# Performance work log

Measured on AMD Instinct MI355X. Metric: run time of the kernel, lower is better.

Reference implementation:

```python
import jax, jax.numpy as jnp
import numpy as np
from jax import lax
from jax.scipy.special import logsumexp

B, T, C = 512, 512, 64


def setup_inputs() -> dict:
    key = jax.random.key(0)
    k1, k2, k3, k4, k5 = jax.random.split(key, 5)
    emissions = jax.random.normal(k1, (B, T, C), dtype=jnp.float32)
    tags = jax.random.randint(k2, (B, T), 0, C, dtype=jnp.int32)
    mask = jnp.ones((B, T), dtype=jnp.int32)
    transitions = jax.random.normal(k3, (C, C), dtype=jnp.float32)
    start_transitions = jax.random.normal(k4, (C,), dtype=jnp.float32)
    end_transitions = jax.random.normal(k5, (C,), dtype=jnp.float32)
    return {"emissions": emissions, "tags": tags, "mask": mask,
            "transitions": transitions, "start_transitions": start_transitions,
            "end_transitions": end_transitions}


def _log_partition(emissions, maskb, transitions, start_transitions, end_transitions):
    # forward algorithm: lp [B,C] carried over T-1 steps
    lp0 = start_transitions[None, :] + emissions[:, 0]  # [B,C]

    def step(lp, xs):
        emit_t, mask_t = xs  # [B,C], [B]
        # score[b,i,j] = lp[b,i] + trans[i,j] + emit[b,j]
        score = lp[:, :, None] + transitions[None, :, :] + emit_t[:, None, :]
        lp_next = logsumexp(score, axis=1)  # [B,C]
        lp = jnp.where(mask_t[:, None], lp_next, lp)
        return lp, None

    xs = (jnp.swapaxes(emissions[:, 1:], 0, 1), jnp.swapaxes(maskb[:, 1:], 0, 1))
    lp, _ = lax.scan(step, lp0, xs)
    return logsumexp(lp + end_transitions[None, :], axis=1)  # [B]


def _joint_score(emissions, tags, mask, maskb, transitions, start_transitions, end_transitions):
    b_idx = jnp.arange(emissions.shape[0])
    score0 = start_transitions[tags[:, 0]] + emissions[b_idx, 0, tags[:, 0]]  # [B]
    trans = transitions[tags[:, :-1], tags[:, 1:]]  # [B,T-1]
    emit = jnp.take_along_axis(emissions, tags[:, :, None], axis=2)[:, :, 0]  # [B,T]
    step_scores = jnp.where(maskb[:, 1:], trans + emit[:, 1:], 0.0)
    last_idx = jnp.sum(mask, axis=1).astype(jnp.int32) - 1
    last_tags = tags[b_idx, last_idx]
    return score0 + jnp.sum(step_scores, axis=1) + end_transitions[last_tags]


def reference(emissions, tags, mask, transitions, start_transitions, end_transitions):
    maskb = mask.astype(bool)
    log_denominator = _log_partition(emissions, maskb, transitions, start_transitions, end_transitions)
    log_numerator = _joint_score(emissions, tags, mask, maskb, transitions, start_transitions, end_transitions)
    return jnp.mean(log_denominator - log_numerator)
```

## Files before the change

kernel.cpp:

```cpp
#include <hip/hip_runtime.h>

#define Bn 512
#define Tn 512
#define Cn 64


template <int CTRL>
__device__ __forceinline__ float fmax_dpp(const float v) {
    const int o = __builtin_amdgcn_update_dpp(__float_as_int(v), __float_as_int(v),
                                              CTRL, 0xF, 0xF, false);
    return fmaxf(v, __int_as_float(o));
}

__device__ __forceinline__ float wave_max64(float v) {
    v = fmax_dpp<0x0B1>(v);
    v = fmax_dpp<0x04E>(v);
    v = fmax_dpp<0x141>(v);
    v = fmax_dpp<0x140>(v);
    v = fmax_dpp<0x142>(v);
    v = fmax_dpp<0x143>(v);
    return __int_as_float(__builtin_amdgcn_readlane(__float_as_int(v), 63));
}

__device__ __forceinline__ float bcast_dot64(const float a, const float* __restrict__ w) {
    const int ai = __float_as_int(a);
    float acc0 = 0.f, acc1 = 0.f, acc2 = 0.f, acc3 = 0.f;
#pragma unroll
    for (int i = 0; i < Cn; i += 4) {
        const float b0 = __int_as_float(__builtin_amdgcn_ds_bpermute(4 * (i + 0), ai));
        const float b1 = __int_as_float(__builtin_amdgcn_ds_bpermute(4 * (i + 1), ai));
        const float b2 = __int_as_float(__builtin_amdgcn_ds_bpermute(4 * (i + 2), ai));
        const float b3 = __int_as_float(__builtin_amdgcn_ds_bpermute(4 * (i + 3), ai));
        acc0 = fmaf(b0, w[i + 0], acc0);
        acc1 = fmaf(b1, w[i + 1], acc1);
        acc2 = fmaf(b2, w[i + 2], acc2);
        acc3 = fmaf(b3, w[i + 3], acc3);
    }
    return (acc0 + acc1) + (acc2 + acc3);
}

__global__ __launch_bounds__(64, 1) void crf_half_kernel(
    const float* __restrict__ emissions,
    const int*   __restrict__ tags,
    const int*   __restrict__ mask,
    const float* __restrict__ transitions,
    const float* __restrict__ start_t,
    const float* __restrict__ end_t,
    float*       __restrict__ ws_alpha,
    float*       __restrict__ ws_beta,
    float*       __restrict__ ws_lsF,
    float*       __restrict__ ws_lsB,
    float*       __restrict__ ws_num)
{
    const int  blk = blockIdx.x;
    const bool fwd = blk < Bn;
    const int  bt  = blk & (Bn - 1);
    const int  j   = threadIdx.x;

    const float* em  = emissions + (size_t)bt * Tn * Cn + j;
    const float* em0 = emissions + (size_t)bt * Tn * Cn;
    const int*   mk  = mask + bt * Tn;
    const int*   tg  = tags + bt * Tn;

    if (fwd) {
        float nsum = 0.f;
        int   mcnt = 0;
        for (int t = j; t < Tn; t += 64) {
            const int tag_t = tg[t];
            const int m_t   = mk[t];
            mcnt += m_t;
            if (t >= 1 && m_t) {
                const int tag_p = tg[t - 1];
                nsum += transitions[tag_p * Cn + tag_t] + em0[t * Cn + tag_t];
            }
        }
#pragma unroll
        for (int off = 32; off > 0; off >>= 1) {
            nsum += __shfl_xor(nsum, off, 64);
            mcnt += __shfl_xor(mcnt, off, 64);
        }

        float w[Cn];
#pragma unroll
        for (int i = 0; i < Cn; ++i) w[i] = __expf(transitions[i * Cn + j]);
#pragma unroll
        for (int i = 0; i < Cn; ++i) asm volatile("" : "+v"(w[i]));

        float lp0 = start_t[j] + em[0];
        const float m0 = wave_max64(lp0);
        float log_scale = m0;
        float a_self = __expf(lp0 - m0);
        float c_pend = 1.0f;

        float cur_e[4];
        int   cur_m[4];
#pragma unroll
        for (int k = 0; k < 4; ++k) {
            cur_e[k] = em[(size_t)(1 + k) * Cn];
            cur_m[k] = mk[1 + k];
        }

        for (int g = 0; g < 64; ++g) {
            float nxt_e[4];
            int   nxt_m[4];
#pragma unroll
            for (int k = 0; k < 4; ++k) {
                const int t = 4 * g + 5 + k;
                nxt_e[k] = em[(size_t)t * Cn];
                nxt_m[k] = mk[t];
            }
            float ex[4];
#pragma unroll
            for (int k = 0; k < 4; ++k) ex[k] = __expf(cur_e[k]);

#pragma unroll
            for (int k = 0; k < 4; ++k) {
                float s = bcast_dot64(a_self, w) * ex[k];
                if (!cur_m[k]) s = a_self;
                if (k == 0) {
                    s *= c_pend;
                    c_pend = 1.0f;
                }
                if (k == 3) {
                    const float mx = wave_max64(s);
                    c_pend = __builtin_amdgcn_rcpf(mx);
                    log_scale += __logf(mx);
                }
                a_self = s;
            }
#pragma unroll
            for (int k = 0; k < 4; ++k) {
                cur_e[k] = nxt_e[k];
                cur_m[k] = nxt_m[k];
            }
        }

        a_self *= c_pend;
        ws_alpha[bt * Cn + j] = a_self;
        if (j == 0) {
            ws_lsF[bt] = log_scale;
            const int t0 = tg[0];
            const int tl = tg[mcnt - 1];
            ws_num[bt] = start_t[t0] + em0[t0] + nsum + end_t[tl];
        }
    } else {
        float w[Cn];
#pragma unroll
        for (int i = 0; i < Cn; ++i) w[i] = __expf(transitions[j * Cn + i]);
#pragma unroll
        for (int i = 0; i < Cn; ++i) asm volatile("" : "+v"(w[i]));

        float lp0 = end_t[j];
        const float m0 = wave_max64(lp0);
        float log_scale = m0;
        float b_self = __expf(lp0 - m0);
        float c_pend = 1.0f;

        float cur_e[4];
        int   cur_m[4];
#pragma unroll
        for (int k = 0; k < 4; ++k) {
            const int u = Tn - 1 - k;
            cur_e[k] = em[(size_t)u * Cn];
            cur_m[k] = mk[u];
        }

        for (int g = 0; g < 64; ++g) {
            float nxt_e[4];
            int   nxt_m[4];
#pragma unroll
            for (int k = 0; k < 4; ++k) {
                const int u = Tn - 5 - 4 * g - k;
                nxt_e[k] = em[(size_t)u * Cn];
                nxt_m[k] = mk[u];
            }
            float ex[4];
#pragma unroll
            for (int k = 0; k < 4; ++k) ex[k] = __expf(cur_e[k]);

#pragma unroll
            for (int k = 0; k < 4; ++k) {
                const int s_idx = 4 * g + k;
                if (s_idx < Tn / 2 - 1) {
                    const float wval = b_self * ex[k];
                    float s = bcast_dot64(wval, w);
                    if (!cur_m[k]) s = b_self;
                    if (k == 0) {
                        s *= c_pend;
                        c_pend = 1.0f;
                    }
                    if (k == 3) {
                        const float mx = wave_max64(s);
                        c_pend = __builtin_amdgcn_rcpf(mx);
                        log_scale += __logf(mx);
                    }
                    b_self = s;
                }
            }
#pragma unroll
            for (int k = 0; k < 4; ++k) {
                cur_e[k] = nxt_e[k];
                cur_m[k] = nxt_m[k];
            }
        }

        b_self *= c_pend;
        ws_beta[bt * Cn + j] = b_self;
        if (j == 0) ws_lsB[bt] = log_scale;
    }
}

__global__ __launch_bounds__(1024) void crf_combine_kernel(
    const float* __restrict__ ws_alpha,
    const float* __restrict__ ws_beta,
    const float* __restrict__ ws_lsF,
    const float* __restrict__ ws_lsB,
    const float* __restrict__ ws_num,
    float*       __restrict__ out)
{
    const int wv = threadIdx.x >> 6;
    const int j  = threadIdx.x & 63;
    const int bt = blockIdx.x * 16 + wv;

    __shared__ float part[16];

    float v = ws_alpha[bt * Cn + j] * ws_beta[bt * Cn + j];
#pragma unroll
    for (int off = 32; off > 0; off >>= 1) v += __shfl_xor(v, off, 64);
    if (j == 0) {
        part[wv] = ws_lsF[bt] + ws_lsB[bt] + __logf(v) - ws_num[bt];
    }
    __syncthreads();
    if (threadIdx.x < 64) {
        float p = (j < 16) ? part[j] : 0.f;
#pragma unroll
        for (int off = 32; off > 0; off >>= 1) p += __shfl_xor(p, off, 64);
        if (j == 0) atomicAdd(out, p * (1.0f / Bn));
    }
}

__global__ void crf_zero_kernel(float* out) { out[0] = 0.f; }

extern "C" void kernel_launch(void* const* d_in, const int* in_sizes, int n_in,
                              void* d_out, int out_size, void* d_ws, size_t ws_size,
                              hipStream_t stream)
{
    const float* emissions   = (const float*)d_in[0];
    const int*   tags        = (const int*)d_in[1];
    const int*   mask        = (const int*)d_in[2];
    const float* transitions = (const float*)d_in[3];
    const float* start_t     = (const float*)d_in[4];
    const float* end_t       = (const float*)d_in[5];

    float* ws       = (float*)d_ws;
    float* ws_alpha = ws;
    float* ws_beta  = ws_alpha + Bn * Cn;
    float* ws_lsF   = ws_beta + Bn * Cn;
    float* ws_lsB   = ws_lsF + Bn;
    float* ws_num   = ws_lsB + Bn;

    crf_zero_kernel<<<1, 1, 0, stream>>>((float*)d_out);
    crf_half_kernel<<<2 * Bn, Cn, 0, stream>>>(emissions, tags, mask, transitions,
                                               start_t, end_t,
                                               ws_alpha, ws_beta, ws_lsF, ws_lsB, ws_num);
    crf_combine_kernel<<<Bn / 16, 1024, 0, stream>>>(ws_alpha, ws_beta, ws_lsF, ws_lsB,
                                                     ws_num, (float*)d_out);
}
```

Before: 171.3 us.

## Replace bpermute broadcast dot with DPP row-rotate systolic matvec and fold zero kernel

Swaps the 64 ds_bpermute broadcasts per step of the 64x64 matvec for a DPP row-rotate scheme. Each lane rotates its value within 16-lane rows, and three extra cross-row copies come from swizzle and shfl_xor. Transition weights are exp'd into LDS and gathered per lane in the matching permuted order. The separate zero-init kernel is also folded into the main kernel. This targets LDS-permute latency on the serial recurrence, at the cost of a more intricate weight layout that has to match the DPP/swizzle lane mapping exactly.

```diff
diff --git a/kernel.cpp b/kernel.cpp
--- a/kernel.cpp
+++ b/kernel.cpp
@@ -22,21 +22,60 @@
     return __int_as_float(__builtin_amdgcn_readlane(__float_as_int(v), 63));
 }
 
-__device__ __forceinline__ float bcast_dot64(const float a, const float* __restrict__ w) {
-    const int ai = __float_as_int(a);
-    float acc0 = 0.f, acc1 = 0.f, acc2 = 0.f, acc3 = 0.f;
-#pragma unroll
-    for (int i = 0; i < Cn; i += 4) {
-        const float b0 = __int_as_float(__builtin_amdgcn_ds_bpermute(4 * (i + 0), ai));
-        const float b1 = __int_as_float(__builtin_amdgcn_ds_bpermute(4 * (i + 1), ai));
-        const float b2 = __int_as_float(__builtin_amdgcn_ds_bpermute(4 * (i + 2), ai));
-        const float b3 = __int_as_float(__builtin_amdgcn_ds_bpermute(4 * (i + 3), ai));
-        acc0 = fmaf(b0, w[i + 0], acc0);
-        acc1 = fmaf(b1, w[i + 1], acc1);
-        acc2 = fmaf(b2, w[i + 2], acc2);
-        acc3 = fmaf(b3, w[i + 3], acc3);
-    }
-    return (acc0 + acc1) + (acc2 + acc3);
+template <int CTRL>
+__device__ __forceinline__ float dppf(const float v) {
+    return __int_as_float(__builtin_amdgcn_update_dpp(
+        __float_as_int(v), __float_as_int(v), CTRL, 0xF, 0xF, false));
+}
+
+__device__ __forceinline__ void phase_acc(const float vp, const float* __restrict__ wp,
+                                          float* __restrict__ A) {
+    A[0] = fmaf(vp,              wp[0],  A[0]);
+    A[1] = fmaf(dppf<0x121>(vp), wp[1],  A[1]);
+    A[2] = fmaf(dppf<0x122>(vp), wp[2],  A[2]);
+    A[3] = fmaf(dppf<0x123>(vp), wp[3],  A[3]);
+    A[4] = fmaf(dppf<0x124>(vp), wp[4],  A[4]);
+    A[5] = fmaf(dppf<0x125>(vp), wp[5],  A[5]);
+    A[6] = fmaf(dppf<0x126>(vp), wp[6],  A[6]);
+    A[7] = fmaf(dppf<0x127>(vp), wp[7],  A[7]);
+    A[0] = fmaf(dppf<0x128>(vp), wp[8],  A[0]);
+    A[1] = fmaf(dppf<0x129>(vp), wp[9],  A[1]);
+    A[2] = fmaf(dppf<0x12A>(vp), wp[10], A[2]);
+    A[3] = fmaf(dppf<0x12B>(vp), wp[11], A[3]);
+    A[4] = fmaf(dppf<0x12C>(vp), wp[12], A[4]);
+    A[5] = fmaf(dppf<0x12D>(vp), wp[13], A[5]);
+    A[6] = fmaf(dppf<0x12E>(vp), wp[14], A[6]);
+    A[7] = fmaf(dppf<0x12F>(vp), wp[15], A[7]);
+}
+
+__device__ __forceinline__ float systolic_dot(const float v, const float* __restrict__ w) {
+    const float v16 = __int_as_float(__builtin_amdgcn_ds_swizzle(__float_as_int(v), 0x401F));
+    const float v32 = __shfl_xor(v, 32, 64);
+    const float v48 = __int_as_float(__builtin_amdgcn_ds_swizzle(__float_as_int(v32), 0x401F));
+
+    float A[8];
+    A[0] = v               * w[0];
+    A[1] = dppf<0x121>(v)  * w[1];
+    A[2] = dppf<0x122>(v)  * w[2];
+    A[3] = dppf<0x123>(v)  * w[3];
+    A[4] = dppf<0x124>(v)  * w[4];
+    A[5] = dppf<0x125>(v)  * w[5];
+    A[6] = dppf<0x126>(v)  * w[6];
+    A[7] = dppf<0x127>(v)  * w[7];
+    A[0] = fmaf(dppf<0x128>(v), w[8],  A[0]);
+    A[1] = fmaf(dppf<0x129>(v), w[9],  A[1]);
+    A[2] = fmaf(dppf<0x12A>(v), w[10], A[2]);
+    A[3] = fmaf(dppf<0x12B>(v), w[11], A[3]);
+    A[4] = fmaf(dppf<0x12C>(v), w[12], A[4]);
+    A[5] = fmaf(dppf<0x12D>(v), w[13], A[5]);
+    A[6] = fmaf(dppf<0x12E>(v), w[14], A[6]);
+    A[7] = fmaf(dppf<0x12F>(v), w[15], A[7]);
+
+    phase_acc(v16, w + 16, A);
+    phase_acc(v32, w + 32, A);
+    phase_acc(v48, w + 48, A);
+
+    return ((A[0] + A[1]) + (A[2] + A[3])) + ((A[4] + A[5]) + (A[6] + A[7]));
 }
 
 __global__ __launch_bounds__(64, 1) void crf_half_kernel(
@@ -50,17 +89,45 @@
     float*       __restrict__ ws_beta,
     float*       __restrict__ ws_lsF,
     float*       __restrict__ ws_lsB,
-    float*       __restrict__ ws_num)
+    float*       __restrict__ ws_num,
+    float*       __restrict__ out)
 {
     const int  blk = blockIdx.x;
     const bool fwd = blk < Bn;
     const int  bt  = blk & (Bn - 1);
     const int  j   = threadIdx.x;
 
+    if (blk == 0 && j == 0) out[0] = 0.f;
+
     const float* em  = emissions + (size_t)bt * Tn * Cn + j;
     const float* em0 = emissions + (size_t)bt * Tn * Cn;
     const int*   mk  = mask + bt * Tn;
     const int*   tg  = tags + bt * Tn;
+
+    __shared__ float lW[Cn * Cn];
+#pragma unroll 8
+    for (int i = 0; i < Cn; ++i)
+        lW[i * Cn + j] = __expf(transitions[i * Cn + j]);
+    __builtin_amdgcn_wave_barrier();
+
+    float w[Cn];
+    if (fwd) {
+#pragma unroll
+        for (int p = 0; p < 4; ++p)
+#pragma unroll
+            for (int r = 0; r < 16; ++r) {
+                const int i = ((j & 48) ^ (p << 4)) | ((j + r) & 15);
+                w[p * 16 + r] = lW[i * Cn + j];
+            }
+    } else {
+#pragma unroll
+        for (int p = 0; p < 4; ++p)
+#pragma unroll
+            for (int r = 0; r < 16; ++r) {
+                const int i = ((j & 48) ^ (p << 4)) | ((j + r) & 15);
+                w[p * 16 + r] = lW[j * Cn + i];
+            }
+    }
 
     if (fwd) {
         float nsum = 0.f;
@@ -80,12 +147,6 @@
             mcnt += __shfl_xor(mcnt, off, 64);
         }
 
-        float w[Cn];
-#pragma unroll
-        for (int i = 0; i < Cn; ++i) w[i] = __expf(transitions[i * Cn + j]);
-#pragma unroll
-        for (int i = 0; i < Cn; ++i) asm volatile("" : "+v"(w[i]));
-
         float lp0 = start_t[j] + em[0];
         const float m0 = wave_max64(lp0);
         float log_scale = m0;
@@ -115,7 +176,7 @@
 
 #pragma unroll
             for (int k = 0; k < 4; ++k) {
-                float s = bcast_dot64(a_self, w) * ex[k];
+                float s = systolic_dot(a_self, w) * ex[k];
                 if (!cur_m[k]) s = a_self;
                 if (k == 0) {
                     s *= c_pend;
@@ -144,12 +205,6 @@
             ws_num[bt] = start_t[t0] + em0[t0] + nsum + end_t[tl];
         }
     } else {
-        float w[Cn];
-#pragma unroll
-        for (int i = 0; i < Cn; ++i) w[i] = __expf(transitions[j * Cn + i]);
-#pragma unroll
-        for (int i = 0; i < Cn; ++i) asm volatile("" : "+v"(w[i]));
-
         float lp0 = end_t[j];
         const float m0 = wave_max64(lp0);
         float log_scale = m0;
@@ -183,7 +238,7 @@
                 const int s_idx = 4 * g + k;
                 if (s_idx < Tn / 2 - 1) {
                     const float wval = b_self * ex[k];
-                    float s = bcast_dot64(wval, w);
+                    float s = systolic_dot(wval, w);
                     if (!cur_m[k]) s = b_self;
                     if (k == 0) {
                         s *= c_pend;
@@ -239,8 +294,6 @@
     }
 }
 
-__global__ void crf_zero_kernel(float* out) { out[0] = 0.f; }
-
 extern "C" void kernel_launch(void* const* d_in, const int* in_sizes, int n_in,
                               void* d_out, int out_size, void* d_ws, size_t ws_size,
                               hipStream_t stream)
@@ -259,10 +312,10 @@
     float* ws_lsB   = ws_lsF + Bn;
     float* ws_num   = ws_lsB + Bn;
 
-    crf_zero_kernel<<<1, 1, 0, stream>>>((float*)d_out);
     crf_half_kernel<<<2 * Bn, Cn, 0, stream>>>(emissions, tags, mask, transitions,
                                                start_t, end_t,
-                                               ws_alpha, ws_beta, ws_lsF, ws_lsB, ws_num);
+                                               ws_alpha, ws_beta, ws_lsF, ws_lsB, ws_num,
+                                               (float*)d_out);
     crf_combine_kernel<<<Bn / 16, 1024, 0, stream>>>(ws_alpha, ws_beta, ws_lsF, ws_lsB,
                                                      ws_num, (float*)d_out);
 }
```

Result: slower. 199.9 us (+16.7%).

## Split CRF recursion across two waves with LDS broadcast and halved dot products

Applied to the files above, without the earlier changes.

Each sequence block now uses 128 threads (two waves) instead of one. Each lane owns one output state and half of the 64-term reduction, and the partial sums are combined with a cross-half shuffle. The previous state vector goes through a double-buffered shared-memory array read as float4, replacing 64 ds_bpermute broadcasts per step. The per-group rescale max is computed from that buffered vector, and the zero-init kernel is folded into the main kernel. The trade-off is a __syncthreads barrier on every time step and twice the thread count per block.

```diff
diff --git a/kernel.cpp b/kernel.cpp
--- a/kernel.cpp
+++ b/kernel.cpp
@@ -4,6 +4,8 @@
 #define Tn 512
 #define Cn 64
 
+
+typedef float f4 __attribute__((ext_vector_type(4)));
 
 template <int CTRL>
 __device__ __forceinline__ float fmax_dpp(const float v) {
@@ -22,24 +24,47 @@
     return __int_as_float(__builtin_amdgcn_readlane(__float_as_int(v), 63));
 }
 
-__device__ __forceinline__ float bcast_dot64(const float a, const float* __restrict__ w) {
-    const int ai = __float_as_int(a);
-    float acc0 = 0.f, acc1 = 0.f, acc2 = 0.f, acc3 = 0.f;
-#pragma unroll
-    for (int i = 0; i < Cn; i += 4) {
-        const float b0 = __int_as_float(__builtin_amdgcn_ds_bpermute(4 * (i + 0), ai));
-        const float b1 = __int_as_float(__builtin_amdgcn_ds_bpermute(4 * (i + 1), ai));
-        const float b2 = __int_as_float(__builtin_amdgcn_ds_bpermute(4 * (i + 2), ai));
-        const float b3 = __int_as_float(__builtin_amdgcn_ds_bpermute(4 * (i + 3), ai));
-        acc0 = fmaf(b0, w[i + 0], acc0);
-        acc1 = fmaf(b1, w[i + 1], acc1);
-        acc2 = fmaf(b2, w[i + 2], acc2);
-        acc3 = fmaf(b3, w[i + 3], acc3);
-    }
-    return (acc0 + acc1) + (acc2 + acc3);
-}
-
-__global__ __launch_bounds__(64, 1) void crf_half_kernel(
+#define READ_BC(rb)                                                        \
+    const f4* ap_ = (const f4*)(&abuf[(rb)][h << 5]);                      \
+    const f4 b0_ = ap_[0], b1_ = ap_[1], b2_ = ap_[2], b3_ = ap_[3],       \
+             b4_ = ap_[4], b5_ = ap_[5], b6_ = ap_[6], b7_ = ap_[7];
+
+#define MAX_FROM_BC(dst)                                                   \
+    float dst;                                                             \
+    {                                                                      \
+        f4 t0_ = __builtin_elementwise_max(b0_, b1_);                      \
+        f4 t1_ = __builtin_elementwise_max(b2_, b3_);                      \
+        f4 t2_ = __builtin_elementwise_max(b4_, b5_);                      \
+        f4 t3_ = __builtin_elementwise_max(b6_, b7_);                      \
+        t0_ = __builtin_elementwise_max(t0_, t1_);                         \
+        t2_ = __builtin_elementwise_max(t2_, t3_);                         \
+        t0_ = __builtin_elementwise_max(t0_, t2_);                         \
+        dst = fmaxf(fmaxf(t0_.x, t0_.y), fmaxf(t0_.z, t0_.w));             \
+    }
+
+#define DOT_FROM_BC(dst)                                                   \
+    float dst;                                                             \
+    {                                                                      \
+        float a0_ = b0_.x * wreg[0],  a1_ = b0_.y * wreg[1];               \
+        float a2_ = b0_.z * wreg[2],  a3_ = b0_.w * wreg[3];               \
+        a0_ = fmaf(b1_.x, wreg[4],  a0_); a1_ = fmaf(b1_.y, wreg[5],  a1_);\
+        a2_ = fmaf(b1_.z, wreg[6],  a2_); a3_ = fmaf(b1_.w, wreg[7],  a3_);\
+        a0_ = fmaf(b2_.x, wreg[8],  a0_); a1_ = fmaf(b2_.y, wreg[9],  a1_);\
+        a2_ = fmaf(b2_.z, wreg[10], a2_); a3_ = fmaf(b2_.w, wreg[11], a3_);\
+        a0_ = fmaf(b3_.x, wreg[12], a0_); a1_ = fmaf(b3_.y, wreg[13], a1_);\
+        a2_ = fmaf(b3_.z, wreg[14], a2_); a3_ = fmaf(b3_.w, wreg[15], a3_);\
+        a0_ = fmaf(b4_.x, wreg[16], a0_); a1_ = fmaf(b4_.y, wreg[17], a1_);\
+        a2_ = fmaf(b4_.z, wreg[18], a2_); a3_ = fmaf(b4_.w, wreg[19], a3_);\
+        a0_ = fmaf(b5_.x, wreg[20], a0_); a1_ = fmaf(b5_.y, wreg[21], a1_);\
+        a2_ = fmaf(b5_.z, wreg[22], a2_); a3_ = fmaf(b5_.w, wreg[23], a3_);\
+        a0_ = fmaf(b6_.x, wreg[24], a0_); a1_ = fmaf(b6_.y, wreg[25], a1_);\
+        a2_ = fmaf(b6_.z, wreg[26], a2_); a3_ = fmaf(b6_.w, wreg[27], a3_);\
+        a0_ = fmaf(b7_.x, wreg[28], a0_); a1_ = fmaf(b7_.y, wreg[29], a1_);\
+        a2_ = fmaf(b7_.z, wreg[30], a2_); a3_ = fmaf(b7_.w, wreg[31], a3_);\
+        dst = (a0_ + a1_) + (a2_ + a3_);                                   \
+    }
+
+__global__ __launch_bounds__(128) void crf_half_kernel(
     const float* __restrict__ emissions,
     const int*   __restrict__ tags,
     const int*   __restrict__ mask,
@@ -50,165 +75,178 @@
     float*       __restrict__ ws_beta,
     float*       __restrict__ ws_lsF,
     float*       __restrict__ ws_lsB,
-    float*       __restrict__ ws_num)
+    float*       __restrict__ ws_num,
+    float*       __restrict__ out)
 {
-    const int  blk = blockIdx.x;
-    const bool fwd = blk < Bn;
-    const int  bt  = blk & (Bn - 1);
-    const int  j   = threadIdx.x;
-
-    const float* em  = emissions + (size_t)bt * Tn * Cn + j;
+    const int  blk  = blockIdx.x;
+    const bool fwd  = blk < Bn;
+    const int  bt   = blk & (Bn - 1);
+    const int  tid  = threadIdx.x;
+    const int  wv   = tid >> 6;
+    const int  l    = tid & 63;
+    const int  h    = l >> 5;
+    const int  ownj = (wv << 5) | (l & 31);
+
+    if (blk == 0 && tid == 0) out[0] = 0.f;
+
+    __shared__ __align__(16) float abuf[2][Cn];
+
+    const float* em  = emissions + (size_t)bt * Tn * Cn + ownj;
     const float* em0 = emissions + (size_t)bt * Tn * Cn;
     const int*   mk  = mask + bt * Tn;
     const int*   tg  = tags + bt * Tn;
 
+    float wreg[32];
     if (fwd) {
-        float nsum = 0.f;
-        int   mcnt = 0;
-        for (int t = j; t < Tn; t += 64) {
-            const int tag_t = tg[t];
-            const int m_t   = mk[t];
-            mcnt += m_t;
-            if (t >= 1 && m_t) {
-                const int tag_p = tg[t - 1];
-                nsum += transitions[tag_p * Cn + tag_t] + em0[t * Cn + tag_t];
-            }
+#pragma unroll
+        for (int m = 0; m < 32; ++m)
+            wreg[m] = __expf(transitions[(h * 32 + m) * Cn + ownj]);
+    } else {
+#pragma unroll
+        for (int m = 0; m < 32; ++m)
+            wreg[m] = __expf(transitions[ownj * Cn + h * 32 + m]);
+    }
+
+    float log_scale, self;
+
+    if (fwd) {
+        const float lp_l = start_t[l] + em0[l];
+        const float m0   = wave_max64(lp_l);
+        log_scale = m0;
+        self = __expf(start_t[ownj] + em0[ownj] - m0);
+
+        abuf[0][ownj] = self;
+        __syncthreads();
+
+        float cE[4]; int cM[4];
+#pragma unroll
+        for (int k = 0; k < 4; ++k) { cE[k] = em[(size_t)(1 + k) * Cn]; cM[k] = mk[1 + k]; }
+
+#pragma unroll 1
+        for (int g = 0; g < 64; ++g) {
+            float nE[4]; int nM[4];
+#pragma unroll
+            for (int k = 0; k < 4; ++k) {
+                const int t = 4 * g + 5 + k;
+                nE[k] = em[(size_t)t * Cn]; nM[k] = mk[t];
+            }
+            float ex[4];
+#pragma unroll
+            for (int k = 0; k < 4; ++k) ex[k] = __expf(cE[k]);
+
+#pragma unroll
+            for (int k = 0; k < 4; ++k) {
+                const int rb = k & 1;
+                READ_BC(rb);
+                float c_ = 1.0f;
+                if (k == 0 && g > 0) {
+                    MAX_FROM_BC(mxl_);
+                    const float mx_ = fmaxf(mxl_, __shfl_xor(mxl_, 32, 64));
+                    c_ = __builtin_amdgcn_rcpf(mx_);
+                    log_scale += __logf(mx_);
+                }
+                DOT_FROM_BC(part_);
+                float s = (part_ + __shfl_xor(part_, 32, 64)) * ex[k];
+                if (!cM[k]) s = self;
+                if (k == 0) s *= c_;
+                self = s;
+                abuf[rb ^ 1][ownj] = s;
+                __syncthreads();
+            }
+#pragma unroll
+            for (int k = 0; k < 4; ++k) { cE[k] = nE[k]; cM[k] = nM[k]; }
         }
-#pragma unroll
-        for (int off = 32; off > 0; off >>= 1) {
-            nsum += __shfl_xor(nsum, off, 64);
-            mcnt += __shfl_xor(mcnt, off, 64);
-        }
-
-        float w[Cn];
-#pragma unroll
-        for (int i = 0; i < Cn; ++i) w[i] = __expf(transitions[i * Cn + j]);
-#pragma unroll
-        for (int i = 0; i < Cn; ++i) asm volatile("" : "+v"(w[i]));
-
-        float lp0 = start_t[j] + em[0];
-        const float m0 = wave_max64(lp0);
-        float log_scale = m0;
-        float a_self = __expf(lp0 - m0);
-        float c_pend = 1.0f;
-
-        float cur_e[4];
-        int   cur_m[4];
-#pragma unroll
-        for (int k = 0; k < 4; ++k) {
-            cur_e[k] = em[(size_t)(1 + k) * Cn];
-            cur_m[k] = mk[1 + k];
-        }
-
-        for (int g = 0; g < 64; ++g) {
-            float nxt_e[4];
-            int   nxt_m[4];
-#pragma unroll
-            for (int k = 0; k < 4; ++k) {
-                const int t = 4 * g + 5 + k;
-                nxt_e[k] = em[(size_t)t * Cn];
-                nxt_m[k] = mk[t];
-            }
-            float ex[4];
-#pragma unroll
-            for (int k = 0; k < 4; ++k) ex[k] = __expf(cur_e[k]);
-
-#pragma unroll
-            for (int k = 0; k < 4; ++k) {
-                float s = bcast_dot64(a_self, w) * ex[k];
-                if (!cur_m[k]) s = a_self;
-                if (k == 0) {
-                    s *= c_pend;
-                    c_pend = 1.0f;
-                }
-                if (k == 3) {
-                    const float mx = wave_max64(s);
-                    c_pend = __builtin_amdgcn_rcpf(mx);
-                    log_scale += __logf(mx);
-                }
-                a_self = s;
-            }
-#pragma unroll
-            for (int k = 0; k < 4; ++k) {
-                cur_e[k] = nxt_e[k];
-                cur_m[k] = nxt_m[k];
-            }
-        }
-
-        a_self *= c_pend;
-        ws_alpha[bt * Cn + j] = a_self;
-        if (j == 0) {
-            ws_lsF[bt] = log_scale;
-            const int t0 = tg[0];
-            const int tl = tg[mcnt - 1];
-            ws_num[bt] = start_t[t0] + em0[t0] + nsum + end_t[tl];
+
+        if (l < 32) ws_alpha[bt * Cn + ownj] = self;
+
+        if (wv == 0) {
+            float nsum = 0.f; int mcnt = 0;
+            for (int t = l; t < Tn; t += 64) {
+                const int tag_t = tg[t];
+                const int m_t   = mk[t];
+                mcnt += m_t;
+                if (t >= 1 && m_t)
+                    nsum += transitions[tg[t - 1] * Cn + tag_t] + em0[t * Cn + tag_t];
+            }
+#pragma unroll
+            for (int off = 32; off > 0; off >>= 1) {
+                nsum += __shfl_xor(nsum, off, 64);
+                mcnt += __shfl_xor(mcnt, off, 64);
+            }
+            if (l == 0) {
+                ws_lsF[bt] = log_scale;
+                const int t0 = tg[0];
+                const int tl = tg[mcnt - 1];
+                ws_num[bt] = start_t[t0] + em0[t0] + nsum + end_t[tl];
+            }
         }
     } else {
-        float w[Cn];
-#pragma unroll
-        for (int i = 0; i < Cn; ++i) w[i] = __expf(transitions[j * Cn + i]);
-#pragma unroll
-        for (int i = 0; i < Cn; ++i) asm volatile("" : "+v"(w[i]));
-
-        float lp0 = end_t[j];
-        const float m0 = wave_max64(lp0);
-        float log_scale = m0;
-        float b_self = __expf(lp0 - m0);
-        float c_pend = 1.0f;
-
-        float cur_e[4];
-        int   cur_m[4];
+        const float lp_l = end_t[l];
+        const float m0   = wave_max64(lp_l);
+        log_scale = m0;
+        self = __expf(end_t[ownj] - m0);
+
+        float eN[4], exC[4]; int mC[4], mN[4];
 #pragma unroll
         for (int k = 0; k < 4; ++k) {
-            const int u = Tn - 1 - k;
-            cur_e[k] = em[(size_t)u * Cn];
-            cur_m[k] = mk[u];
+            exC[k] = __expf(em[(size_t)(Tn - 1 - k) * Cn]);
+            eN[k]  = em[(size_t)(Tn - 5 - k) * Cn];
+            mC[k]  = mk[Tn - 1 - k];
+            mN[k]  = mk[Tn - 5 - k];
         }
 
+        abuf[0][ownj] = self * exC[0];
+        __syncthreads();
+
+#pragma unroll 1
         for (int g = 0; g < 64; ++g) {
-            float nxt_e[4];
-            int   nxt_m[4];
-#pragma unroll
-            for (int k = 0; k < 4; ++k) {
-                const int u = Tn - 5 - 4 * g - k;
-                nxt_e[k] = em[(size_t)u * Cn];
-                nxt_m[k] = mk[u];
-            }
-            float ex[4];
-#pragma unroll
-            for (int k = 0; k < 4; ++k) ex[k] = __expf(cur_e[k]);
-
-#pragma unroll
-            for (int k = 0; k < 4; ++k) {
-                const int s_idx = 4 * g + k;
-                if (s_idx < Tn / 2 - 1) {
-                    const float wval = b_self * ex[k];
-                    float s = bcast_dot64(wval, w);
-                    if (!cur_m[k]) s = b_self;
-                    if (k == 0) {
-                        s *= c_pend;
-                        c_pend = 1.0f;
+            float eF[4]; int mF[4];
+#pragma unroll
+            for (int k = 0; k < 4; ++k) {
+                const int u = 503 - 4 * g - k;
+                eF[k] = em[(size_t)u * Cn]; mF[k] = mk[u];
+            }
+            float exN[4];
+#pragma unroll
+            for (int k = 0; k < 4; ++k) exN[k] = __expf(eN[k]);
+
+#pragma unroll
+            for (int k = 0; k < 4; ++k) {
+                const int sidx = 4 * g + k;
+                if (sidx < Tn / 2 - 1) {
+                    const int rb = k & 1;
+                    READ_BC(rb);
+                    float c_ = 1.0f;
+                    if (k == 0 && g > 0) {
+                        MAX_FROM_BC(mxl_);
+                        const float mx_ = fmaxf(mxl_, __shfl_xor(mxl_, 32, 64));
+                        c_ = __builtin_amdgcn_rcpf(mx_);
+                        log_scale += __logf(mx_);
                     }
-                    if (k == 3) {
-                        const float mx = wave_max64(s);
-                        c_pend = __builtin_amdgcn_rcpf(mx);
-                        log_scale += __logf(mx);
-                    }
-                    b_self = s;
+                    DOT_FROM_BC(part_);
+                    float s = part_ + __shfl_xor(part_, 32, 64);
+                    if (!mC[k]) s = self;
+                    if (k == 0) s *= c_;
+                    self = s;
+                    const float exn = (k < 3) ? exC[k + 1] : exN[0];
+                    abuf[rb ^ 1][ownj] = s * exn;
+                    __syncthreads();
                 }
             }
 #pragma unroll
             for (int k = 0; k < 4; ++k) {
-                cur_e[k] = nxt_e[k];
-                cur_m[k] = nxt_m[k];
+                exC[k] = exN[k]; eN[k] = eF[k]; mC[k] = mN[k]; mN[k] = mF[k];
             }
         }
 
-        b_self *= c_pend;
-        ws_beta[bt * Cn + j] = b_self;
-        if (j == 0) ws_lsB[bt] = log_scale;
-    }
-}
+        if (l < 32) ws_beta[bt * Cn + ownj] = self;
+        if (tid == 0) ws_lsB[bt] = log_scale;
+    }
+}
+
+#undef READ_BC
+#undef MAX_FROM_BC
+#undef DOT_FROM_BC
 
 __global__ __launch_bounds__(1024) void crf_combine_kernel(
     const float* __restrict__ ws_alpha,
@@ -239,8 +277,6 @@
     }
 }
 
-__global__ void crf_zero_kernel(float* out) { out[0] = 0.f; }
-
 extern "C" void kernel_launch(void* const* d_in, const int* in_sizes, int n_in,
                               void* d_out, int out_size, void* d_ws, size_t ws_size,
                               hipStream_t stream)
@@ -259,10 +295,10 @@
     float* ws_lsB   = ws_lsF + Bn;
     float* ws_num   = ws_lsB + Bn;
 
-    crf_zero_kernel<<<1, 1, 0, stream>>>((float*)d_out);
-    crf_half_kernel<<<2 * Bn, Cn, 0, stream>>>(emissions, tags, mask, transitions,
-                                               start_t, end_t,
-                                               ws_alpha, ws_beta, ws_lsF, ws_lsB, ws_num);
+    crf_half_kernel<<<2 * Bn, 128, 0, stream>>>(emissions, tags, mask, transitions,
+                                                start_t, end_t,
+                                                ws_alpha, ws_beta, ws_lsF, ws_lsB, ws_num,
+                                                (float*)d_out);
     crf_combine_kernel<<<Bn / 16, 1024, 0, stream>>>(ws_alpha, ws_beta, ws_lsF, ws_lsB,
                                                      ws_num, (float*)d_out);
 }
```

New measurement: 182.6 us. +6.6%, slower.
